# Performance work log

Hardware: AMD Instinct MI355X
Metric: run time of the kernel (lower is better)

Reference implementation:

```python
import jax, jax.numpy as jnp
import numpy as np

D_MODEL = 1024
NUM_HEADS = 16
HEAD_DIM = D_MODEL // NUM_HEADS
R = 1.0
LAM = 0.1
CLIP_MIN = -15.0
CLIP_MAX = 15.0
EPS = 1e-9


def setup_inputs() -> dict:
    key = jax.random.key(0)
    k1, k2 = jax.random.split(key, 2)
    B, S = 2, 2048
    x = jax.random.normal(k1, (B, S, D_MODEL), dtype=jnp.float32)
    # NonNeg-constrained dense kernel -> nonnegative uniform init (small scale)
    W = jax.random.uniform(k2, (D_MODEL, D_MODEL), dtype=jnp.float32) * 0.02
    b = jnp.zeros((D_MODEL,), dtype=jnp.float32)
    d_q = jnp.ones((D_MODEL,), dtype=jnp.float32)
    d_k = jnp.ones((D_MODEL,), dtype=jnp.float32)
    d_v = jnp.ones((D_MODEL,), dtype=jnp.float32)
    return {"x": x, "W": W, "b": b, "d_q": d_q, "d_k": d_k, "d_v": d_v}


def _convex_r_softmax(z):
    z = jnp.clip(z, CLIP_MIN, CLIP_MAX)
    numerator = jax.nn.relu(jnp.exp(z - R) + LAM * z)
    denominator = jnp.sum(numerator, axis=-1, keepdims=True) + EPS
    return numerator / denominator


def reference(x, W, b, d_q, d_k, d_v):
    B, S, _ = x.shape
    x_proj = x @ W + b                      # [B, S, D]
    # diagonal scaling then split heads: [B, H, S, Dh]
    def heads(t):
        return t.reshape(B, S, NUM_HEADS, HEAD_DIM).transpose(0, 2, 1, 3)
    Q = heads(x_proj * d_q)
    K = heads(x_proj * d_k)
    V = heads(x_proj * d_v)
    scores = jnp.einsum('bhqd,bhkd->bhqk', Q, K)   # [B, H, S, S]
    attn = _convex_r_softmax(scores)
    out = jnp.einsum('bhqk,bhkd->bhqd', attn, V)   # [B, H, S, Dh]
    return out.transpose(0, 2, 1, 3).reshape(B, S, D_MODEL)
```

## Files before the change

### kernel.cpp

```cpp
#include <hip/hip_runtime.h>
#include <math.h>

#define D_MODEL   1024
#define NUM_HEADS 16
#define HEAD_DIM  64
#define S_LEN     2048
#define BATCH     2
#define M_TOT     (BATCH * S_LEN)

typedef __attribute__((ext_vector_type(8))) short short8;
typedef __attribute__((ext_vector_type(4))) short short4v;
typedef __attribute__((ext_vector_type(4))) float f32x4;

static __device__ __forceinline__ short f2bf(float f) {
    unsigned u = __builtin_bit_cast(unsigned, f);
    unsigned r = (u + 0x7FFFu + ((u >> 16) & 1u)) >> 16;
    return (short)r;
}
static __device__ __forceinline__ float bf2f(short s) {
    return __builtin_bit_cast(float, ((unsigned)(unsigned short)s) << 16);
}

typedef __attribute__((address_space(3))) void lds_v;
typedef const __attribute__((address_space(1))) void glb_v;
static __device__ __forceinline__ void gll16(const void* g, void* l) {
    __builtin_amdgcn_global_load_lds((glb_v*)g, (lds_v*)l, 16, 0, 0);
}


__global__ __launch_bounds__(256) void cvt_xw_kernel(
    const float* __restrict__ x, short* __restrict__ xb,
    const float* __restrict__ W, short* __restrict__ wt)
{
    __shared__ short T[64][72];
    const int bx = blockIdx.x;
    if (bx < 2048) {
        int i = (bx * 256 + threadIdx.x) * 8;
        float4 a = *(const float4*)(x + i);
        float4 b = *(const float4*)(x + i + 4);
        short8 o;
        o[0] = f2bf(a.x); o[1] = f2bf(a.y); o[2] = f2bf(a.z); o[3] = f2bf(a.w);
        o[4] = f2bf(b.x); o[5] = f2bf(b.y); o[6] = f2bf(b.z); o[7] = f2bf(b.w);
        *(short8*)(xb + i) = o;
    } else {
        const int t = bx - 2048;
        const int tid = threadIdx.x;
        const int k0 = (t >> 4) * 64, n0 = (t & 15) * 64;
        const int r = tid >> 4, c4 = (tid & 15) * 4;
        #pragma unroll
        for (int i = 0; i < 4; i++) {
            int kr = r + 16 * i;
            float4 v = *(const float4*)(W + (size_t)(k0 + kr) * D_MODEL + n0 + c4);
            short4v s;
            s[0] = f2bf(v.x); s[1] = f2bf(v.y); s[2] = f2bf(v.z); s[3] = f2bf(v.w);
            *(short4v*)&T[kr][c4] = s;
        }
        __syncthreads();
        const int n = tid >> 2, kb = (tid & 3) * 16;
        short tmp[16];
        #pragma unroll
        for (int j = 0; j < 16; j++) tmp[j] = T[kb + j][n];
        *(short8*)(wt + (size_t)(n0 + n) * D_MODEL + k0 + kb)     = *(short8*)&tmp[0];
        *(short8*)(wt + (size_t)(n0 + n) * D_MODEL + k0 + kb + 8) = *(short8*)&tmp[8];
    }
}

__global__ __launch_bounds__(256) void gemm_qkv_kernel(
    const short* __restrict__ xb, const short* __restrict__ wt,
    const float* __restrict__ bias, const float* __restrict__ dq,
    const float* __restrict__ dk, const float* __restrict__ dv,
    short* __restrict__ Q, short* __restrict__ K, short* __restrict__ Vt)
{
    __shared__ __attribute__((aligned(16))) short lds[24576];

    const int tid  = threadIdx.x;
    const int w    = tid >> 6, l = tid & 63;
    const int quad = l >> 4,  c = l & 15;
    const int n0 = blockIdx.x * 128, m0 = blockIdx.y * 64;
    const int wm = (w & 1) * 32, wn = (w >> 1) * 64;
    short* As = lds;
    short* Bs = lds + 8192;

    const int sub  = l >> 4;
    const int slot = l & 15;

    f32x4 acc[2][4];
    #pragma unroll
    for (int mi = 0; mi < 2; mi++)
        #pragma unroll
        for (int ni = 0; ni < 4; ni++) acc[mi][ni] = (f32x4){0.f, 0.f, 0.f, 0.f};

    for (int k0 = 0; k0 < D_MODEL; k0 += 128) {
        __syncthreads();
        #pragma unroll
        for (int i = 0; i < 4; i++) {
            int rbase = 16 * w + 4 * i;
            int row = rbase + sub;
            int ss = slot ^ (row & 15);
            gll16(xb + (size_t)(m0 + row) * D_MODEL + k0 + ss * 8, As + rbase * 128);
        }
        #pragma unroll
        for (int i = 0; i < 8; i++) {
            int rbase = 32 * w + 4 * i;
            int row = rbase + sub;
            int ss = slot ^ (row & 15);
            gll16(wt + (size_t)(n0 + row) * D_MODEL + k0 + ss * 8, Bs + rbase * 128);
        }
        __syncthreads();
        #pragma unroll
        for (int kh = 0; kh < 4; kh++) {
            const int sx = (kh * 4 + quad) ^ c;
            short8 af[2], bf[4];
            #pragma unroll
            for (int mi = 0; mi < 2; mi++)
                af[mi] = *(const short8*)&As[(wm + 16 * mi + c) * 128 + sx * 8];
            #pragma unroll
            for (int ni = 0; ni < 4; ni++)
                bf[ni] = *(const short8*)&Bs[(wn + 16 * ni + c) * 128 + sx * 8];
            #pragma unroll
            for (int mi = 0; mi < 2; mi++)
                #pragma unroll
                for (int ni = 0; ni < 4; ni++)
                    acc[mi][ni] = __builtin_amdgcn_mfma_f32_16x16x32_bf16(
                        af[mi], bf[ni], acc[mi][ni], 0, 0, 0);
        }
    }

    __syncthreads();
    const int b      = m0 >> 11;
    const int s_base = m0 & 2047;
    const int h      = (n0 + wn) >> 6;

    float biasv[4], dqv[4], dkv[4], dvv[4];
    #pragma unroll
    for (int ni = 0; ni < 4; ni++) {
        int n_g = n0 + wn + 16 * ni + c;
        biasv[ni] = bias[n_g]; dqv[ni] = dq[n_g];
        dkv[ni] = dk[n_g];     dvv[ni] = dv[n_g];
    }

    short* E = lds;
    #pragma unroll
    for (int mi = 0; mi < 2; mi++) {
        #pragma unroll
        for (int ni = 0; ni < 4; ni++) {
            short4v vv;
            #pragma unroll
            for (int r = 0; r < 4; r++) {
                float xv = acc[mi][ni][r] + biasv[ni];
                int s = s_base + wm + 16 * mi + 4 * quad + r;
                size_t off = (((size_t)(b * NUM_HEADS + h) * S_LEN + s) << 6) + (16 * ni + c);
                Q[off] = f2bf(xv * dqv[ni]);
                K[off] = f2bf(xv * dkv[ni]);
                vv[r]  = f2bf(xv * dvv[ni]);
            }
            int n_l = wn + 16 * ni + c;
            int m_l = wm + 16 * mi + 4 * quad;
            *(short4v*)&E[n_l * 72 + m_l] = vv;
        }
    }
    __syncthreads();
    {
        const int n_l = tid >> 1, mh = (tid & 1) * 32;
        const int h2 = (n0 + n_l) >> 6;
        const int dh = n_l & 63;
        short* dst = Vt + ((size_t)(b * NUM_HEADS + h2) * HEAD_DIM + dh) * S_LEN + s_base;
        #pragma unroll
        for (int ch = 0; ch < 4; ch++) {
            short8 v = *(const short8*)&E[n_l * 72 + mh + ch * 8];
            *(short8*)(dst + mh + ch * 8) = v;
        }
    }
}

__global__ __launch_bounds__(256, 4) void attn_split_kernel(
    const short* __restrict__ Q, const short* __restrict__ K,
    const short* __restrict__ Vt, short* __restrict__ Opart,
    float* __restrict__ dpart)
{
    __shared__ __attribute__((aligned(16))) short lds[8192 + 4 * 32 * 88];

    const int tid  = threadIdx.x;
    const int w    = tid >> 6, l = tid & 63;
    const int quad = l >> 4,  c = l & 15;
    const int cx   = c & 7;
    const int qt    = blockIdx.x >> 1;
    const int split = blockIdx.x & 1;
    const int q0 = qt * 128;
    const int h  = blockIdx.y, b = blockIdx.z;
    const size_t bh = (size_t)(b * NUM_HEADS + h);
    const short* Qh  = Q  + bh * S_LEN * HEAD_DIM;
    const short* Kh  = K  + bh * S_LEN * HEAD_DIM;
    const short* Vth = Vt + bh * HEAD_DIM * S_LEN;

    short* Ks = lds;
    short* Vs = lds + 4096;
    short* Ps = lds + 8192 + w * (32 * 88);

    const int srow  = l >> 3;
    const int sslot = (l & 7) ^ srow;

    short8 qf0[2], qf1[2];
    {
        const short* qp0 = Qh + (size_t)(q0 + 32 * w + c) * 64 + quad * 8;
        const short* qp1 = qp0 + 16 * 64;
        qf0[0] = *(const short8*)(qp0);
        qf0[1] = *(const short8*)(qp0 + 32);
        qf1[0] = *(const short8*)(qp1);
        qf1[1] = *(const short8*)(qp1 + 32);
    }

    short8 ones;
    #pragma unroll
    for (int j = 0; j < 8; j++) ones[j] = (short)0x3F80;

    f32x4 o0[4], o1[4], d0a, d1a;
    #pragma unroll
    for (int i = 0; i < 4; i++) {
        o0[i] = (f32x4){0.f, 0.f, 0.f, 0.f};
        o1[i] = (f32x4){0.f, 0.f, 0.f, 0.f};
    }
    d0a = (f32x4){0.f, 0.f, 0.f, 0.f};
    d1a = (f32x4){0.f, 0.f, 0.f, 0.f};

    const int kt_beg = split * (S_LEN / 128);
    for (int kt = kt_beg; kt < kt_beg + S_LEN / 128; kt++) {
        const int k0 = kt * 64;
        __syncthreads();
        #pragma unroll
        for (int i = 0; i < 2; i++) {
            int rbase = 16 * w + 8 * i;
            int row = rbase + srow;
            gll16(Kh + (size_t)(k0 + row) * 64 + sslot * 8, Ks + rbase * 64);
            gll16(Vth + (size_t)row * S_LEN + k0 + sslot * 8, Vs + rbase * 64);
        }
        __syncthreads();

        #pragma unroll
        for (int nh = 0; nh < 2; nh++) {
            f32x4 s0[2], s1[2];
            #pragma unroll
            for (int nn = 0; nn < 2; nn++) {
                s0[nn] = (f32x4){0.f, 0.f, 0.f, 0.f};
                s1[nn] = (f32x4){0.f, 0.f, 0.f, 0.f};
            }
            #pragma unroll
            for (int hh = 0; hh < 2; hh++) {
                const int sx = (hh * 4 + quad) ^ cx;
                #pragma unroll
                for (int nn = 0; nn < 2; nn++) {
                    const int n = 2 * nh + nn;
                    short8 kf = *(const short8*)&Ks[(16 * n + c) * 64 + sx * 8];
                    s0[nn] = __builtin_amdgcn_mfma_f32_16x16x32_bf16(kf, qf0[hh], s0[nn], 0, 0, 0);
                    s1[nn] = __builtin_amdgcn_mfma_f32_16x16x32_bf16(kf, qf1[hh], s1[nn], 0, 0, 0);
                }
            }
            #pragma unroll
            for (int nn = 0; nn < 2; nn++) {
                const int n = 2 * nh + nn;
                float nm[4];
                #pragma unroll
                for (int r = 0; r < 4; r++) {
                    float z = __builtin_amdgcn_fmed3f(s0[nn][r], -15.0f, 15.0f);
                    float e = __builtin_amdgcn_exp2f(
                        __builtin_fmaf(z, 1.4426950408889634f, -1.4426950408889634f));
                    nm[r] = fmaxf(__builtin_fmaf(z, 0.1f, e), 0.0f);
                }
                unsigned p0 = __builtin_amdgcn_perm(
                    __builtin_bit_cast(unsigned, nm[1]) + 0x8000u,
                    __builtin_bit_cast(unsigned, nm[0]) + 0x8000u, 0x07060302u);
                unsigned p1 = __builtin_amdgcn_perm(
                    __builtin_bit_cast(unsigned, nm[3]) + 0x8000u,
                    __builtin_bit_cast(unsigned, nm[2]) + 0x8000u, 0x07060302u);
                uint2 pr; pr.x = p0; pr.y = p1;
                *(uint2*)&Ps[c * 88 + 16 * n + 4 * quad] = pr;
            }
            #pragma unroll
            for (int nn = 0; nn < 2; nn++) {
                const int n = 2 * nh + nn;
                float nm[4];
                #pragma unroll
                for (int r = 0; r < 4; r++) {
                    float z = __builtin_amdgcn_fmed3f(s1[nn][r], -15.0f, 15.0f);
                    float e = __builtin_amdgcn_exp2f(
                        __builtin_fmaf(z, 1.4426950408889634f, -1.4426950408889634f));
                    nm[r] = fmaxf(__builtin_fmaf(z, 0.1f, e), 0.0f);
                }
                unsigned p0 = __builtin_amdgcn_perm(
                    __builtin_bit_cast(unsigned, nm[1]) + 0x8000u,
                    __builtin_bit_cast(unsigned, nm[0]) + 0x8000u, 0x07060302u);
                unsigned p1 = __builtin_amdgcn_perm(
                    __builtin_bit_cast(unsigned, nm[3]) + 0x8000u,
                    __builtin_bit_cast(unsigned, nm[2]) + 0x8000u, 0x07060302u);
                uint2 pr; pr.x = p0; pr.y = p1;
                *(uint2*)&Ps[(16 + c) * 88 + 16 * n + 4 * quad] = pr;
            }
        }

        #pragma unroll
        for (int kh = 0; kh < 2; kh++) {
            short8 pf0 = *(const short8*)&Ps[c * 88 + 32 * kh + 8 * quad];
            short8 pf1 = *(const short8*)&Ps[(16 + c) * 88 + 32 * kh + 8 * quad];
            const int sx = (kh * 4 + quad) ^ cx;
            #pragma unroll
            for (int n2 = 0; n2 < 4; n2++) {
                short8 vf = *(const short8*)&Vs[(16 * n2 + c) * 64 + sx * 8];
                o0[n2] = __builtin_amdgcn_mfma_f32_16x16x32_bf16(pf0, vf, o0[n2], 0, 0, 0);
                o1[n2] = __builtin_amdgcn_mfma_f32_16x16x32_bf16(pf1, vf, o1[n2], 0, 0, 0);
            }
            d0a = __builtin_amdgcn_mfma_f32_16x16x32_bf16(pf0, ones, d0a, 0, 0, 0);
            d1a = __builtin_amdgcn_mfma_f32_16x16x32_bf16(pf1, ones, d1a, 0, 0, 0);
        }
    }

    short* Op = Opart + ((((size_t)split * BATCH + b) * NUM_HEADS + h) * 16 + qt) * (128 * 64);
    float* dp = dpart + ((((size_t)split * BATCH + b) * NUM_HEADS + h) * 16 + qt) * 128;

    #pragma unroll
    for (int r = 0; r < 4; r++) {
        int row0 = 32 * w + 4 * quad + r;
        #pragma unroll
        for (int n2 = 0; n2 < 4; n2++) {
            Op[row0 * 64 + 16 * n2 + c]        = f2bf(o0[n2][r]);
            Op[(row0 + 16) * 64 + 16 * n2 + c] = f2bf(o1[n2][r]);
        }
        if (c == 0) {
            dp[row0]      = d0a[r];
            dp[row0 + 16] = d1a[r];
        }
    }
}

__global__ __launch_bounds__(256) void combine_kernel(
    const short* __restrict__ Opart, const float* __restrict__ dpart,
    float* __restrict__ out)
{
    const int gid = blockIdx.x * 256 + threadIdx.x;
    const int row = gid >> 4;
    const int col = (gid & 15) * 4;
    float d = dpart[row] + dpart[65536 + row] + 1e-9f;
    float inv = 1.0f / d;
    short4v a  = *(const short4v*)(Opart + (size_t)gid * 4);
    short4v b2 = *(const short4v*)(Opart + 4194304 + (size_t)gid * 4);
    const int b = row >> 15;
    const int h = (row >> 11) & 15;
    const int s = row & 2047;
    float4 r;
    r.x = (bf2f(a[0]) + bf2f(b2[0])) * inv;
    r.y = (bf2f(a[1]) + bf2f(b2[1])) * inv;
    r.z = (bf2f(a[2]) + bf2f(b2[2])) * inv;
    r.w = (bf2f(a[3]) + bf2f(b2[3])) * inv;
    *(float4*)(out + ((size_t)(b * S_LEN + s) << 10) + (h << 6) + col) = r;
}

__global__ __launch_bounds__(256) void attn2_kernel(
    const short* __restrict__ Q, const short* __restrict__ K,
    const short* __restrict__ Vt, float* __restrict__ out)
{
    __shared__ __attribute__((aligned(16))) short lds[8192 + 4 * 32 * 88];

    const int tid  = threadIdx.x;
    const int w    = tid >> 6, l = tid & 63;
    const int quad = l >> 4,  c = l & 15;
    const int cx   = c & 7;
    const int q0 = blockIdx.x * 128;
    const int h  = blockIdx.y, b = blockIdx.z;
    const size_t bh = (size_t)(b * NUM_HEADS + h);
    const short* Qh  = Q  + bh * S_LEN * HEAD_DIM;
    const short* Kh  = K  + bh * S_LEN * HEAD_DIM;
    const short* Vth = Vt + bh * HEAD_DIM * S_LEN;

    short* Ks = lds;
    short* Vs = lds + 4096;
    short* Ps = lds + 8192 + w * (32 * 88);

    const int srow  = l >> 3;
    const int sslot = (l & 7) ^ srow;

    short8 qf0[2], qf1[2];
    {
        const short* qp0 = Qh + (size_t)(q0 + 32 * w + c) * 64 + quad * 8;
        const short* qp1 = qp0 + 16 * 64;
        qf0[0] = *(const short8*)(qp0);
        qf0[1] = *(const short8*)(qp0 + 32);
        qf1[0] = *(const short8*)(qp1);
        qf1[1] = *(const short8*)(qp1 + 32);
    }

    f32x4 o0[4], o1[4];
    #pragma unroll
    for (int i = 0; i < 4; i++) {
        o0[i] = (f32x4){0.f, 0.f, 0.f, 0.f};
        o1[i] = (f32x4){0.f, 0.f, 0.f, 0.f};
    }
    float dnm0 = 0.0f, dnm1 = 0.0f;

    for (int kt = 0; kt < S_LEN / 64; kt++) {
        const int k0 = kt * 64;
        __syncthreads();
        #pragma unroll
        for (int i = 0; i < 2; i++) {
            int rbase = 16 * w + 8 * i;
            int row = rbase + srow;
            gll16(Kh + (size_t)(k0 + row) * 64 + sslot * 8, Ks + rbase * 64);
            gll16(Vth + (size_t)row * S_LEN + k0 + sslot * 8, Vs + rbase * 64);
        }
        __syncthreads();

        f32x4 s0[4], s1[4];
        #pragma unroll
        for (int n = 0; n < 4; n++) {
            s0[n] = (f32x4){0.f, 0.f, 0.f, 0.f};
            s1[n] = (f32x4){0.f, 0.f, 0.f, 0.f};
        }
        #pragma unroll
        for (int hh = 0; hh < 2; hh++) {
            const int sx = (hh * 4 + quad) ^ cx;
            #pragma unroll
            for (int n = 0; n < 4; n++) {
                short8 kf = *(const short8*)&Ks[(16 * n + c) * 64 + sx * 8];
                s0[n] = __builtin_amdgcn_mfma_f32_16x16x32_bf16(kf, qf0[hh], s0[n], 0, 0, 0);
                s1[n] = __builtin_amdgcn_mfma_f32_16x16x32_bf16(kf, qf1[hh], s1[n], 0, 0, 0);
            }
        }

        #pragma unroll
        for (int n = 0; n < 4; n++) {
            float nm[4];
            #pragma unroll
            for (int r = 0; r < 4; r++) {
                float z = __builtin_amdgcn_fmed3f(s0[n][r], -15.0f, 15.0f);
                float e = __builtin_amdgcn_exp2f(
                    __builtin_fmaf(z, 1.4426950408889634f, -1.4426950408889634f));
                float num = fmaxf(__builtin_fmaf(z, 0.1f, e), 0.0f);
                dnm0 += num;
                nm[r] = num;
            }
            unsigned p0 = __builtin_amdgcn_perm(
                __builtin_bit_cast(unsigned, nm[1]) + 0x8000u,
                __builtin_bit_cast(unsigned, nm[0]) + 0x8000u, 0x07060302u);
            unsigned p1 = __builtin_amdgcn_perm(
                __builtin_bit_cast(unsigned, nm[3]) + 0x8000u,
                __builtin_bit_cast(unsigned, nm[2]) + 0x8000u, 0x07060302u);
            uint2 pr; pr.x = p0; pr.y = p1;
            *(uint2*)&Ps[c * 88 + 16 * n + 4 * quad] = pr;
        }
        #pragma unroll
        for (int n = 0; n < 4; n++) {
            float nm[4];
            #pragma unroll
            for (int r = 0; r < 4; r++) {
                float z = __builtin_amdgcn_fmed3f(s1[n][r], -15.0f, 15.0f);
                float e = __builtin_amdgcn_exp2f(
                    __builtin_fmaf(z, 1.4426950408889634f, -1.4426950408889634f));
                float num = fmaxf(__builtin_fmaf(z, 0.1f, e), 0.0f);
                dnm1 += num;
                nm[r] = num;
            }
            unsigned p0 = __builtin_amdgcn_perm(
                __builtin_bit_cast(unsigned, nm[1]) + 0x8000u,
                __builtin_bit_cast(unsigned, nm[0]) + 0x8000u, 0x07060302u);
            unsigned p1 = __builtin_amdgcn_perm(
                __builtin_bit_cast(unsigned, nm[3]) + 0x8000u,
                __builtin_bit_cast(unsigned, nm[2]) + 0x8000u, 0x07060302u);
            uint2 pr; pr.x = p0; pr.y = p1;
            *(uint2*)&Ps[(16 + c) * 88 + 16 * n + 4 * quad] = pr;
        }

        #pragma unroll
        for (int kh = 0; kh < 2; kh++) {
            short8 pf0 = *(const short8*)&Ps[c * 88 + 32 * kh + 8 * quad];
            short8 pf1 = *(const short8*)&Ps[(16 + c) * 88 + 32 * kh + 8 * quad];
            const int sx = (kh * 4 + quad) ^ cx;
            #pragma unroll
            for (int n2 = 0; n2 < 4; n2++) {
                short8 vf = *(const short8*)&Vs[(16 * n2 + c) * 64 + sx * 8];
                o0[n2] = __builtin_amdgcn_mfma_f32_16x16x32_bf16(pf0, vf, o0[n2], 0, 0, 0);
                o1[n2] = __builtin_amdgcn_mfma_f32_16x16x32_bf16(pf1, vf, o1[n2], 0, 0, 0);
            }
        }
    }

    dnm0 += __shfl_xor(dnm0, 16, 64);
    dnm0 += __shfl_xor(dnm0, 32, 64);
    dnm1 += __shfl_xor(dnm1, 16, 64);
    dnm1 += __shfl_xor(dnm1, 32, 64);

    #pragma unroll
    for (int r = 0; r < 4; r++) {
        float dr0 = __shfl(dnm0, quad * 4 + r, 64);
        float dr1 = __shfl(dnm1, quad * 4 + r, 64);
        float inv0 = 1.0f / (dr0 + 1e-9f);
        float inv1 = 1.0f / (dr1 + 1e-9f);
        int qrow0 = q0 + 32 * w + 4 * quad + r;
        float* op0 = out + ((size_t)(b * S_LEN + qrow0) << 10) + (h << 6) + c;
        float* op1 = op0 + (16 << 10);
        #pragma unroll
        for (int n2 = 0; n2 < 4; n2++) {
            op0[16 * n2] = o0[n2][r] * inv0;
            op1[16 * n2] = o1[n2][r] * inv1;
        }
    }
}

__global__ __launch_bounds__(256, 4) void gemm_xw_kernel(
    const float* __restrict__ x, const float* __restrict__ W,
    const float* __restrict__ bias, float* __restrict__ xp)
{
    __shared__ float Asf[64][36];
    __shared__ float Bsf[32][68];

    const int tid = threadIdx.x;
    const int tx  = tid & 15;
    const int ty  = tid >> 4;
    const int m0  = blockIdx.y * 64;
    const int n0  = blockIdx.x * 64;

    float acc[4][4];
    #pragma unroll
    for (int i = 0; i < 4; i++)
        #pragma unroll
        for (int j = 0; j < 4; j++) acc[i][j] = 0.0f;

    for (int k0 = 0; k0 < D_MODEL; k0 += 32) {
        #pragma unroll
        for (int i = 0; i < 2; i++) {
            int idx = tid + i * 256;
            int r = idx >> 3, c4 = idx & 7;
            *(float4*)(&Asf[r][c4 * 4]) =
                *(const float4*)(x + (size_t)(m0 + r) * D_MODEL + k0 + c4 * 4);
        }
        #pragma unroll
        for (int i = 0; i < 2; i++) {
            int idx = tid + i * 256;
            int r = idx >> 4, c4 = idx & 15;
            *(float4*)(&Bsf[r][c4 * 4]) =
                *(const float4*)(W + (size_t)(k0 + r) * D_MODEL + n0 + c4 * 4);
        }
        __syncthreads();
        #pragma unroll
        for (int k = 0; k < 32; k += 4) {
            float a[4][4];
            #pragma unroll
            for (int i = 0; i < 4; i++) {
                float4 t = *(const float4*)(&Asf[ty + 16 * i][k]);
                a[i][0] = t.x; a[i][1] = t.y; a[i][2] = t.z; a[i][3] = t.w;
            }
            #pragma unroll
            for (int kk = 0; kk < 4; kk++) {
                float4 bv = *(const float4*)(&Bsf[k + kk][tx * 4]);
                #pragma unroll
                for (int i = 0; i < 4; i++) {
                    acc[i][0] += a[i][kk] * bv.x;
                    acc[i][1] += a[i][kk] * bv.y;
                    acc[i][2] += a[i][kk] * bv.z;
                    acc[i][3] += a[i][kk] * bv.w;
                }
            }
        }
        __syncthreads();
    }
    float4 bv = *(const float4*)(bias + n0 + tx * 4);
    #pragma unroll
    for (int i = 0; i < 4; i++) {
        float4 r;
        r.x = acc[i][0] + bv.x; r.y = acc[i][1] + bv.y;
        r.z = acc[i][2] + bv.z; r.w = acc[i][3] + bv.w;
        *(float4*)(xp + (size_t)(m0 + ty + 16 * i) * D_MODEL + n0 + tx * 4) = r;
    }
}

__global__ __launch_bounds__(256, 4) void attn_fb_kernel(
    const float* __restrict__ xp, const float* __restrict__ dq,
    const float* __restrict__ dk, const float* __restrict__ dv,
    float* __restrict__ out)
{
    __shared__ __attribute__((aligned(16))) short lds[13824];

    const int tid  = threadIdx.x;
    const int wave = tid >> 6;
    const int l    = tid & 63;
    const int quad = l >> 4;
    const int c    = l & 15;
    const int q0   = blockIdx.x * 64;
    const int h    = blockIdx.y;
    const int bb   = blockIdx.z;
    const int col0 = h * HEAD_DIM;
    const float* base = xp + (size_t)bb * S_LEN * D_MODEL;

    short* Ks = lds;
    short* Vt = lds + 64 * 72;
    short* Ps = lds + 2 * 64 * 72 + wave * (16 * 72);

    short8 qf[2];
    {
        const int qrow = q0 + wave * 16 + c;
        const float* qp = base + (size_t)qrow * D_MODEL + col0 + quad * 8;
        const float* sp = dq + col0 + quad * 8;
        #pragma unroll
        for (int hh = 0; hh < 2; hh++) {
            float4 v0 = *(const float4*)(qp + 32 * hh);
            float4 v1 = *(const float4*)(qp + 32 * hh + 4);
            float4 s0 = *(const float4*)(sp + 32 * hh);
            float4 s1 = *(const float4*)(sp + 32 * hh + 4);
            qf[hh][0] = f2bf(v0.x * s0.x); qf[hh][1] = f2bf(v0.y * s0.y);
            qf[hh][2] = f2bf(v0.z * s0.z); qf[hh][3] = f2bf(v0.w * s0.w);
            qf[hh][4] = f2bf(v1.x * s1.x); qf[hh][5] = f2bf(v1.y * s1.y);
            qf[hh][6] = f2bf(v1.z * s1.z); qf[hh][7] = f2bf(v1.w * s1.w);
        }
    }

    const int sc4  = 4 * (tid & 15);
    const int srow = tid >> 4;
    const float4 ksc = *(const float4*)(dk + col0 + sc4);
    const int vd = tid & 63;
    const int vg = tid >> 6;
    const float vsc = dv[col0 + vd];

    f32x4 acc_o[4];
    #pragma unroll
    for (int i = 0; i < 4; i++) acc_o[i] = (f32x4){0.f, 0.f, 0.f, 0.f};
    float dnm = 0.0f;

    for (int kt = 0; kt < S_LEN / 64; kt++) {
        const int k0 = kt * 64;
        __syncthreads();

        #pragma unroll
        for (int i = 0; i < 4; i++) {
            int r = srow + 16 * i;
            float4 v = *(const float4*)(base + (size_t)(k0 + r) * D_MODEL + col0 + sc4);
            short4v s;
            s[0] = f2bf(v.x * ksc.x); s[1] = f2bf(v.y * ksc.y);
            s[2] = f2bf(v.z * ksc.z); s[3] = f2bf(v.w * ksc.w);
            *(short4v*)&Ks[r * 72 + sc4] = s;
        }
        #pragma unroll
        for (int p = 0; p < 4; p++) {
            int kb = 16 * p + 4 * vg;
            const float* vp = base + (size_t)(k0 + kb) * D_MODEL + col0 + vd;
            float a0 = vp[0 * D_MODEL], a1 = vp[1 * D_MODEL];
            float a2 = vp[2 * D_MODEL], a3 = vp[3 * D_MODEL];
            short4v s;
            s[0] = f2bf(a0 * vsc); s[1] = f2bf(a1 * vsc);
            s[2] = f2bf(a2 * vsc); s[3] = f2bf(a3 * vsc);
            *(short4v*)&Vt[vd * 72 + kb] = s;
        }
        __syncthreads();

        f32x4 sacc[4];
        #pragma unroll
        for (int n = 0; n < 4; n++) sacc[n] = (f32x4){0.f, 0.f, 0.f, 0.f};
        #pragma unroll
        for (int n = 0; n < 4; n++)
            #pragma unroll
            for (int hh = 0; hh < 2; hh++) {
                short8 kf = *(const short8*)&Ks[(16 * n + c) * 72 + 32 * hh + 8 * quad];
                sacc[n] = __builtin_amdgcn_mfma_f32_16x16x32_bf16(kf, qf[hh], sacc[n], 0, 0, 0);
            }

        #pragma unroll
        for (int n = 0; n < 4; n++) {
            short4v pp;
            #pragma unroll
            for (int r = 0; r < 4; r++) {
                float z = fminf(fmaxf(sacc[n][r], -15.0f), 15.0f);
                float e = __expf(z - 1.0f);
                float num = fmaxf(fmaf(z, 0.1f, e), 0.0f);
                dnm += num;
                pp[r] = f2bf(num);
            }
            *(short4v*)&Ps[c * 72 + 16 * n + 4 * quad] = pp;
        }

        #pragma unroll
        for (int kh = 0; kh < 2; kh++) {
            short8 pf = *(const short8*)&Ps[c * 72 + 32 * kh + 8 * quad];
            #pragma unroll
            for (int n2 = 0; n2 < 4; n2++) {
                short8 vf = *(const short8*)&Vt[(16 * n2 + c) * 72 + 32 * kh + 8 * quad];
                acc_o[n2] = __builtin_amdgcn_mfma_f32_16x16x32_bf16(pf, vf, acc_o[n2], 0, 0, 0);
            }
        }
    }

    dnm += __shfl_xor(dnm, 16, 64);
    dnm += __shfl_xor(dnm, 32, 64);

    #pragma unroll
    for (int r = 0; r < 4; r++) {
        float dr  = __shfl(dnm, quad * 4 + r, 64);
        float inv = 1.0f / (dr + 1e-9f);
        const int qrow = q0 + wave * 16 + quad * 4 + r;
        float* op = out + (size_t)(bb * S_LEN + qrow) * D_MODEL + col0 + c;
        #pragma unroll
        for (int n2 = 0; n2 < 4; n2++)
            op[16 * n2] = acc_o[n2][r] * inv;
    }
}

extern "C" void kernel_launch(void* const* d_in, const int* in_sizes, int n_in,
                              void* d_out, int out_size, void* d_ws, size_t ws_size,
                              hipStream_t stream) {
    const float* x  = (const float*)d_in[0];
    const float* W  = (const float*)d_in[1];
    const float* bias = (const float*)d_in[2];
    const float* dq = (const float*)d_in[3];
    const float* dk = (const float*)d_in[4];
    const float* dv = (const float*)d_in[5];
    float* out = (float*)d_out;

    const size_t XB_B = (size_t)M_TOT * D_MODEL * 2;
    const size_t WT_B = (size_t)D_MODEL * D_MODEL * 2;
    const size_t T_B  = (size_t)BATCH * NUM_HEADS * S_LEN * HEAD_DIM * 2;
    const size_t OP_B = (size_t)2 * 65536 * 64 * 2;
    const size_t DP_B = (size_t)2 * 65536 * 4;
    const size_t NEED1 = XB_B + WT_B + 3 * T_B;
    const size_t NEED2 = NEED1 + OP_B + DP_B;

    if (ws_size >= NEED1) {
        char* p = (char*)d_ws;
        short* xb = (short*)p;             p += XB_B;
        short* wt = (short*)p;             p += WT_B;
        short* Qt = (short*)p;             p += T_B;
        short* Kt = (short*)p;             p += T_B;
        short* Vt = (short*)p;             p += T_B;

        cvt_xw_kernel<<<2048 + 256, 256, 0, stream>>>(x, xb, W, wt);
        dim3 gg(D_MODEL / 128, M_TOT / 64);
        gemm_qkv_kernel<<<gg, 256, 0, stream>>>(xb, wt, bias, dq, dk, dv, Qt, Kt, Vt);

        if (ws_size >= NEED2) {
            short* Opart = (short*)p;      p += OP_B;
            float* dpart = (float*)p;
            dim3 ga(2 * S_LEN / 128, NUM_HEADS, BATCH);
            attn_split_kernel<<<ga, 256, 0, stream>>>(Qt, Kt, Vt, Opart, dpart);
            combine_kernel<<<4096, 256, 0, stream>>>(Opart, dpart, out);
        } else {
            dim3 ga(S_LEN / 128, NUM_HEADS, BATCH);
            attn2_kernel<<<ga, 256, 0, stream>>>(Qt, Kt, Vt, out);
        }
    } else {
        float* xp = (float*)d_ws;
        dim3 g1(D_MODEL / 64, M_TOT / 64);
        gemm_xw_kernel<<<g1, 256, 0, stream>>>(x, W, bias, xp);
        dim3 g2(S_LEN / 64, NUM_HEADS, BATCH);
        attn_fb_kernel<<<g2, 256, 0, stream>>>(xp, dq, dk, dv, out);
    }
}
```

Before: 155.7 us.

## Double-buffer LDS tiles in QKV GEMM and attention kernels with single barrier

Both the QKV projection GEMM and the split attention kernel now double-buffer their shared-memory tiles. The next K-tile is issued via async global-to-LDS loads while the current tile is consumed, with one barrier per iteration instead of two. The GEMM K-step drops from 128 to 64 with a matching 8-slot XOR swizzle, and the attention P scratch row pitch shrinks from 88 to 72 to make room. The attention kernel's LDS grows to about 50KB, which may limit how many blocks fit per CU against its launch bound of 4.

Measured after the change: 160.3 us. 1.03x slower.

```diff
diff --git a/kernel.cpp b/kernel.cpp
--- a/kernel.cpp
+++ b/kernel.cpp
@@ -76,13 +76,12 @@
     const int tid  = threadIdx.x;
     const int w    = tid >> 6, l = tid & 63;
     const int quad = l >> 4,  c = l & 15;
+    const int cx   = c & 7;
     const int n0 = blockIdx.x * 128, m0 = blockIdx.y * 64;
     const int wm = (w & 1) * 32, wn = (w >> 1) * 64;
-    short* As = lds;
-    short* Bs = lds + 8192;
-
-    const int sub  = l >> 4;
-    const int slot = l & 15;
+
+    const int srow  = l >> 3;
+    const int sslot = (l & 7) ^ srow;
 
     f32x4 acc[2][4];
     #pragma unroll
@@ -90,33 +89,40 @@
         #pragma unroll
         for (int ni = 0; ni < 4; ni++) acc[mi][ni] = (f32x4){0.f, 0.f, 0.f, 0.f};
 
-    for (int k0 = 0; k0 < D_MODEL; k0 += 128) {
-        __syncthreads();
+    auto stage = [&](int kt, int bsel) {
+        const int k0 = kt * 64;
+        short* As = lds + bsel * 4096;
+        short* Bs = lds + 8192 + bsel * 8192;
+        #pragma unroll
+        for (int i = 0; i < 2; i++) {
+            int rbase = 16 * w + 8 * i;
+            gll16(xb + (size_t)(m0 + rbase + srow) * D_MODEL + k0 + sslot * 8,
+                  As + rbase * 64);
+        }
         #pragma unroll
         for (int i = 0; i < 4; i++) {
-            int rbase = 16 * w + 4 * i;
-            int row = rbase + sub;
-            int ss = slot ^ (row & 15);
-            gll16(xb + (size_t)(m0 + row) * D_MODEL + k0 + ss * 8, As + rbase * 128);
-        }
-        #pragma unroll
-        for (int i = 0; i < 8; i++) {
-            int rbase = 32 * w + 4 * i;
-            int row = rbase + sub;
-            int ss = slot ^ (row & 15);
-            gll16(wt + (size_t)(n0 + row) * D_MODEL + k0 + ss * 8, Bs + rbase * 128);
-        }
-        __syncthreads();
-        #pragma unroll
-        for (int kh = 0; kh < 4; kh++) {
-            const int sx = (kh * 4 + quad) ^ c;
+            int rbase = 32 * w + 8 * i;
+            gll16(wt + (size_t)(n0 + rbase + srow) * D_MODEL + k0 + sslot * 8,
+                  Bs + rbase * 64);
+        }
+    };
+
+    stage(0, 0);
+    for (int it = 0; it < 16; it++) {
+        __syncthreads();
+        if (it < 15) stage(it + 1, (it + 1) & 1);
+        const short* As = lds + (it & 1) * 4096;
+        const short* Bs = lds + 8192 + (it & 1) * 8192;
+        #pragma unroll
+        for (int kh = 0; kh < 2; kh++) {
+            const int sx = (kh * 4 + quad) ^ cx;
             short8 af[2], bf[4];
             #pragma unroll
             for (int mi = 0; mi < 2; mi++)
-                af[mi] = *(const short8*)&As[(wm + 16 * mi + c) * 128 + sx * 8];
+                af[mi] = *(const short8*)&As[(wm + 16 * mi + c) * 64 + sx * 8];
             #pragma unroll
             for (int ni = 0; ni < 4; ni++)
-                bf[ni] = *(const short8*)&Bs[(wn + 16 * ni + c) * 128 + sx * 8];
+                bf[ni] = *(const short8*)&Bs[(wn + 16 * ni + c) * 64 + sx * 8];
             #pragma unroll
             for (int mi = 0; mi < 2; mi++)
                 #pragma unroll
@@ -178,7 +184,7 @@
     const short* __restrict__ Vt, short* __restrict__ Opart,
     float* __restrict__ dpart)
 {
-    __shared__ __attribute__((aligned(16))) short lds[8192 + 4 * 32 * 88];
+    __shared__ __attribute__((aligned(16))) short lds[25600];
 
     const int tid  = threadIdx.x;
     const int w    = tid >> 6, l = tid & 63;
@@ -193,9 +199,7 @@
     const short* Kh  = K  + bh * S_LEN * HEAD_DIM;
     const short* Vth = Vt + bh * HEAD_DIM * S_LEN;
 
-    short* Ks = lds;
-    short* Vs = lds + 4096;
-    short* Ps = lds + 8192 + w * (32 * 88);
+    short* Ps = lds + 16384 + w * (32 * 72);
 
     const int srow  = l >> 3;
     const int sslot = (l & 7) ^ srow;
@@ -223,10 +227,12 @@
     d0a = (f32x4){0.f, 0.f, 0.f, 0.f};
     d1a = (f32x4){0.f, 0.f, 0.f, 0.f};
 
-    const int kt_beg = split * (S_LEN / 128);
-    for (int kt = kt_beg; kt < kt_beg + S_LEN / 128; kt++) {
+    const int kt_beg = split * 16;
+
+    auto stage = [&](int kt, int bsel) {
         const int k0 = kt * 64;
-        __syncthreads();
+        short* Ks = lds + bsel * 4096;
+        short* Vs = lds + 8192 + bsel * 4096;
         #pragma unroll
         for (int i = 0; i < 2; i++) {
             int rbase = 16 * w + 8 * i;
@@ -234,7 +240,14 @@
             gll16(Kh + (size_t)(k0 + row) * 64 + sslot * 8, Ks + rbase * 64);
             gll16(Vth + (size_t)row * S_LEN + k0 + sslot * 8, Vs + rbase * 64);
         }
-        __syncthreads();
+    };
+
+    stage(kt_beg, 0);
+    for (int it = 0; it < 16; it++) {
+        __syncthreads();
+        if (it < 15) stage(kt_beg + it + 1, (it + 1) & 1);
+        const short* Ks = lds + (it & 1) * 4096;
+        const short* Vs = lds + 8192 + (it & 1) * 4096;
 
         #pragma unroll
         for (int nh = 0; nh < 2; nh++) {
@@ -273,7 +286,7 @@
                     __builtin_bit_cast(unsigned, nm[3]) + 0x8000u,
                     __builtin_bit_cast(unsigned, nm[2]) + 0x8000u, 0x07060302u);
                 uint2 pr; pr.x = p0; pr.y = p1;
-                *(uint2*)&Ps[c * 88 + 16 * n + 4 * quad] = pr;
+                *(uint2*)&Ps[c * 72 + 16 * n + 4 * quad] = pr;
             }
             #pragma unroll
             for (int nn = 0; nn < 2; nn++) {
@@ -293,14 +306,14 @@
                     __builtin_bit_cast(unsigned, nm[3]) + 0x8000u,
                     __builtin_bit_cast(unsigned, nm[2]) + 0x8000u, 0x07060302u);
                 uint2 pr; pr.x = p0; pr.y = p1;
-                *(uint2*)&Ps[(16 + c) * 88 + 16 * n + 4 * quad] = pr;
+                *(uint2*)&Ps[(16 + c) * 72 + 16 * n + 4 * quad] = pr;
             }
         }
 
         #pragma unroll
         for (int kh = 0; kh < 2; kh++) {
-            short8 pf0 = *(const short8*)&Ps[c * 88 + 32 * kh + 8 * quad];
-            short8 pf1 = *(const short8*)&Ps[(16 + c) * 88 + 32 * kh + 8 * quad];
+            short8 pf0 = *(const short8*)&Ps[c * 72 + 32 * kh + 8 * quad];
+            short8 pf1 = *(const short8*)&Ps[(16 + c) * 72 + 32 * kh + 8 * quad];
             const int sx = (kh * 4 + quad) ^ cx;
             #pragma unroll
             for (int n2 = 0; n2 < 4; n2++) {
```

## Shrink QKV GEMM tile to 64x64 with k-step 64 for more blocks

Applied to the files above, without the earlier changes.

Retiles the QKV projection GEMM from 64x128 tiles with a 128-wide K step to 64x64 tiles with a 64-wide K step. This reduces LDS use (48KB down to 16KB), halves the accumulators per wave, and doubles the grid to 1024 blocks, with a launch bound of 4 blocks per CU. The aim is higher occupancy and better filling of the CUs. In exchange, each loaded tile is reused less and there are twice as many K iterations, each ending in a barrier.

Result: no change. 157.1 us (+0.9%).

```diff
diff --git a/kernel.cpp b/kernel.cpp
--- a/kernel.cpp
+++ b/kernel.cpp
@@ -65,62 +65,57 @@
     }
 }
 
-__global__ __launch_bounds__(256) void gemm_qkv_kernel(
+__global__ __launch_bounds__(256, 4) void gemm_qkv_kernel(
     const short* __restrict__ xb, const short* __restrict__ wt,
     const float* __restrict__ bias, const float* __restrict__ dq,
     const float* __restrict__ dk, const float* __restrict__ dv,
     short* __restrict__ Q, short* __restrict__ K, short* __restrict__ Vt)
 {
-    __shared__ __attribute__((aligned(16))) short lds[24576];
+    __shared__ __attribute__((aligned(16))) short lds[8192];
 
     const int tid  = threadIdx.x;
     const int w    = tid >> 6, l = tid & 63;
     const int quad = l >> 4,  c = l & 15;
-    const int n0 = blockIdx.x * 128, m0 = blockIdx.y * 64;
-    const int wm = (w & 1) * 32, wn = (w >> 1) * 64;
+    const int cx   = c & 7;
+    const int n0 = blockIdx.x * 64, m0 = blockIdx.y * 64;
+    const int wm = (w & 1) * 32, wn = (w >> 1) * 32;
     short* As = lds;
-    short* Bs = lds + 8192;
-
-    const int sub  = l >> 4;
-    const int slot = l & 15;
-
-    f32x4 acc[2][4];
+    short* Bs = lds + 4096;
+
+    const int srow  = l >> 3;
+    const int sslot = (l & 7) ^ srow;
+
+    f32x4 acc[2][2];
     #pragma unroll
     for (int mi = 0; mi < 2; mi++)
         #pragma unroll
-        for (int ni = 0; ni < 4; ni++) acc[mi][ni] = (f32x4){0.f, 0.f, 0.f, 0.f};
-
-    for (int k0 = 0; k0 < D_MODEL; k0 += 128) {
-        __syncthreads();
-        #pragma unroll
-        for (int i = 0; i < 4; i++) {
-            int rbase = 16 * w + 4 * i;
-            int row = rbase + sub;
-            int ss = slot ^ (row & 15);
-            gll16(xb + (size_t)(m0 + row) * D_MODEL + k0 + ss * 8, As + rbase * 128);
-        }
-        #pragma unroll
-        for (int i = 0; i < 8; i++) {
-            int rbase = 32 * w + 4 * i;
-            int row = rbase + sub;
-            int ss = slot ^ (row & 15);
-            gll16(wt + (size_t)(n0 + row) * D_MODEL + k0 + ss * 8, Bs + rbase * 128);
-        }
-        __syncthreads();
-        #pragma unroll
-        for (int kh = 0; kh < 4; kh++) {
-            const int sx = (kh * 4 + quad) ^ c;
-            short8 af[2], bf[4];
+        for (int ni = 0; ni < 2; ni++) acc[mi][ni] = (f32x4){0.f, 0.f, 0.f, 0.f};
+
+    for (int k0 = 0; k0 < D_MODEL; k0 += 64) {
+        __syncthreads();
+        #pragma unroll
+        for (int i = 0; i < 2; i++) {
+            int rbase = 16 * w + 8 * i;
+            gll16(xb + (size_t)(m0 + rbase + srow) * D_MODEL + k0 + sslot * 8,
+                  As + rbase * 64);
+            gll16(wt + (size_t)(n0 + rbase + srow) * D_MODEL + k0 + sslot * 8,
+                  Bs + rbase * 64);
+        }
+        __syncthreads();
+        #pragma unroll
+        for (int kh = 0; kh < 2; kh++) {
+            const int sx = (kh * 4 + quad) ^ cx;
+            short8 af[2], bf[2];
             #pragma unroll
             for (int mi = 0; mi < 2; mi++)
-                af[mi] = *(const short8*)&As[(wm + 16 * mi + c) * 128 + sx * 8];
-            #pragma unroll
-            for (int ni = 0; ni < 4; ni++)
-                bf[ni] = *(const short8*)&Bs[(wn + 16 * ni + c) * 128 + sx * 8];
+                af[mi] = *(const short8*)&As[(wm + 16 * mi + c) * 64 + sx * 8];
+            #pragma unroll
+            for (int ni = 0; ni < 2; ni++)
+                bf[ni] = *(const short8*)&Bs[(wn + 16 * ni + c) * 64 + sx * 8];
             #pragma unroll
             for (int mi = 0; mi < 2; mi++)
                 #pragma unroll
-                for (int ni = 0; ni < 4; ni++)
+                for (int ni = 0; ni < 2; ni++)
                     acc[mi][ni] = __builtin_amdgcn_mfma_f32_16x16x32_bf16(
                         af[mi], bf[ni], acc[mi][ni], 0, 0, 0);
         }
@@ -129,11 +124,11 @@
     __syncthreads();
     const int b      = m0 >> 11;
     const int s_base = m0 & 2047;
-    const int h      = (n0 + wn) >> 6;
-
-    float biasv[4], dqv[4], dkv[4], dvv[4];
-    #pragma unroll
-    for (int ni = 0; ni < 4; ni++) {
+    const int h      = n0 >> 6;
+
+    float biasv[2], dqv[2], dkv[2], dvv[2];
+    #pragma unroll
+    for (int ni = 0; ni < 2; ni++) {
         int n_g = n0 + wn + 16 * ni + c;
         biasv[ni] = bias[n_g]; dqv[ni] = dq[n_g];
         dkv[ni] = dk[n_g];     dvv[ni] = dv[n_g];
@@ -143,13 +138,14 @@
     #pragma unroll
     for (int mi = 0; mi < 2; mi++) {
         #pragma unroll
-        for (int ni = 0; ni < 4; ni++) {
+        for (int ni = 0; ni < 2; ni++) {
             short4v vv;
             #pragma unroll
             for (int r = 0; r < 4; r++) {
                 float xv = acc[mi][ni][r] + biasv[ni];
                 int s = s_base + wm + 16 * mi + 4 * quad + r;
-                size_t off = (((size_t)(b * NUM_HEADS + h) * S_LEN + s) << 6) + (16 * ni + c);
+                size_t off = (((size_t)(b * NUM_HEADS + h) * S_LEN + s) << 6)
+                           + (wn + 16 * ni + c);
                 Q[off] = f2bf(xv * dqv[ni]);
                 K[off] = f2bf(xv * dkv[ni]);
                 vv[r]  = f2bf(xv * dvv[ni]);
@@ -161,15 +157,13 @@
     }
     __syncthreads();
     {
-        const int n_l = tid >> 1, mh = (tid & 1) * 32;
-        const int h2 = (n0 + n_l) >> 6;
-        const int dh = n_l & 63;
-        short* dst = Vt + ((size_t)(b * NUM_HEADS + h2) * HEAD_DIM + dh) * S_LEN + s_base;
-        #pragma unroll
-        for (int ch = 0; ch < 4; ch++) {
-            short8 v = *(const short8*)&E[n_l * 72 + mh + ch * 8];
-            *(short8*)(dst + mh + ch * 8) = v;
-        }
+        const int n_l = tid >> 2, mh = (tid & 3) * 16;
+        short* dst = Vt + ((size_t)(b * NUM_HEADS + h) * HEAD_DIM + n_l) * S_LEN
+                        + s_base + mh;
+        short8 v0 = *(const short8*)&E[n_l * 72 + mh];
+        short8 v1 = *(const short8*)&E[n_l * 72 + mh + 8];
+        *(short8*)(dst)     = v0;
+        *(short8*)(dst + 8) = v1;
     }
 }
 
@@ -727,7 +721,7 @@
         short* Vt = (short*)p;             p += T_B;
 
         cvt_xw_kernel<<<2048 + 256, 256, 0, stream>>>(x, xb, W, wt);
-        dim3 gg(D_MODEL / 128, M_TOT / 64);
+        dim3 gg(D_MODEL / 64, M_TOT / 64);
         gemm_qkv_kernel<<<gg, 256, 0, stream>>>(xb, wt, bias, dq, dk, dv, Qt, Kt, Vt);
 
         if (ws_size >= NEED2) {
```
